# Kernel optimization log

Measured on AMD Instinct MI355X. Metric: run time of the kernel, lower is better.

The kernel has to match this reference:

```python
import jax, jax.numpy as jnp
import numpy as np

B, N, C, DK, TOPK = 4, 4096, 256, 64, 8


def setup_inputs() -> dict:
    key = jax.random.key(0)
    k1, k2, k3 = jax.random.split(key, 3)
    x = jax.random.normal(k1, (B, N, C), dtype=jnp.float32)
    # nn.Linear(channels, d_k, bias=False) weights, stored as [C, DK] for x @ W
    W_q = jax.random.normal(k2, (C, DK), dtype=jnp.float32) * (C ** -0.5)
    W_k = jax.random.normal(k3, (C, DK), dtype=jnp.float32) * (C ** -0.5)
    return {"x": x, "W_q": W_q, "W_k": W_k, "top_k": TOPK}


def reference(x, W_q, W_k, top_k):
    d_k = W_q.shape[-1]
    scale = d_k ** -0.5
    Q = x @ W_q                                   # [B, N, DK]
    K = x @ W_k                                   # [B, N, DK]
    S = jnp.einsum('bnd,bmd->bnm', Q, K) * scale  # [B, N, N]
    _, topk_idx = jax.lax.top_k(S, top_k)         # [B, N, top_k]
    n = S.shape[-1]
    # scatter True at top-k column indices per row (mirrors torch scatter_)
    row_mask = lambda idx: jnp.zeros((n,), dtype=bool).at[idx].set(True)
    mask = jax.vmap(jax.vmap(row_mask))(topk_idx)  # [B, N, N] bool
    S_masked = jnp.where(mask, S, -jnp.inf)
    A = jax.nn.softmax(S_masked, axis=-1)
    return A
```

## Files before the change

### kernel.cpp

```cpp
#include <hip/hip_runtime.h>
#include <math.h>

#define NROW 16384
#define NCOL 4096
#define CDIM 256
#define DKDIM 64
#define SCALE 0.125f

typedef float v4f __attribute__((ext_vector_type(4)));
typedef __attribute__((ext_vector_type(8))) short short8v;
typedef __attribute__((ext_vector_type(4))) float f32x4;

__device__ __forceinline__ unsigned mono(float v) {
  unsigned u = __float_as_uint(v);
  unsigned s = (unsigned)(((int)u) >> 31);
  return u ^ (s | 0x80000000u);
}
__device__ __forceinline__ float unmono(unsigned k) {
  unsigned u = (k & 0x80000000u) ? (k ^ 0x80000000u) : ~k;
  return __uint_as_float(u);
}
__device__ __forceinline__ unsigned short f2bf(float f) {
  unsigned u = __float_as_uint(f);
  u += 0x7FFFu + ((u >> 16) & 1u);
  return (unsigned short)(u >> 16);
}
__device__ __forceinline__ unsigned umaxu(unsigned a, unsigned b) { return a > b ? a : b; }

__device__ __forceinline__ void ins8(unsigned tk[8], unsigned& tmin, int& tmpos, unsigned v) {
  #pragma unroll
  for (int j = 0; j < 8; ++j) if (j == tmpos) tk[j] = v;
  tmin = tk[0]; tmpos = 0;
  #pragma unroll
  for (int j = 1; j < 8; ++j) if (tk[j] < tmin) { tmin = tk[j]; tmpos = j; }
}
__device__ __forceinline__ unsigned umax8(const unsigned kv[8]) {
  unsigned a = umaxu(umaxu(kv[0], kv[1]), umaxu(kv[2], kv[3]));
  unsigned b = umaxu(umaxu(kv[4], kv[5]), umaxu(kv[6], kv[7]));
  return umaxu(a, b);
}
__device__ __forceinline__ void seed8r(const unsigned kv[8],
                                       unsigned tk[8], unsigned& tmin, int& tmpos) {
  #pragma unroll
  for (int j = 0; j < 8; ++j) tk[j] = kv[j];
  tmin = tk[0]; tmpos = 0;
  #pragma unroll
  for (int j = 1; j < 8; ++j) if (tk[j] < tmin) { tmin = tk[j]; tmpos = j; }
}
__device__ __forceinline__ void scan8r(const unsigned kvin[8],
                                       unsigned tk[8], unsigned& tmin, int& tmpos) {
  unsigned kv[8];
  #pragma unroll
  for (int j = 0; j < 8; ++j) kv[j] = kvin[j];
  unsigned gm = umax8(kv);
  #pragma unroll
  for (int pass = 0; pass < 2; ++pass) {
    if (__any(gm > tmin)) {
      if (gm > tmin) {
        ins8(tk, tmin, tmpos, gm);
        #pragma unroll
        for (int j = 0; j < 8; ++j) if (kv[j] == gm) kv[j] = 0u;
      }
      gm = umax8(kv);
    }
  }
  if (__any(gm > tmin)) {
    #pragma unroll
    for (int j = 0; j < 8; ++j) if (kv[j] > tmin) ins8(tk, tmin, tmpos, kv[j]);
  }
}
__device__ __forceinline__ void seed8(const unsigned* __restrict__ sp,
                                      unsigned tk[8], unsigned& tmin, int& tmpos) {
  uint4 ka = *(const uint4*)(sp);
  uint4 kb = *(const uint4*)(sp + 4);
  unsigned kv[8] = {ka.x, ka.y, ka.z, ka.w, kb.x, kb.y, kb.z, kb.w};
  seed8r(kv, tk, tmin, tmpos);
}
__device__ __forceinline__ void scan8(const unsigned* __restrict__ sp,
                                      unsigned tk[8], unsigned& tmin, int& tmpos) {
  uint4 ka = *(const uint4*)(sp);
  uint4 kb = *(const uint4*)(sp + 4);
  unsigned kv[8] = {ka.x, ka.y, ka.z, ka.w, kb.x, kb.y, kb.z, kb.w};
  scan8r(kv, tk, tmin, tmpos);
}

__global__ __launch_bounds__(512, 2) void qk_proj(
    const float* __restrict__ x, const float* __restrict__ Wq,
    const float* __restrict__ Wk, float* __restrict__ Qt,
    float* __restrict__ Kt, unsigned short* __restrict__ Qh,
    unsigned short* __restrict__ Kh, float* __restrict__ out) {
  __shared__ float4 xs4[64][65];
  const int t = threadIdx.x;
  const int rb = blockIdx.x;
  {
    const float4* xg = (const float4*)(x + (size_t)rb * 64 * CDIM);
    #pragma unroll
    for (int i = 0; i < 8; ++i) {
      int idx = i * 512 + t;
      xs4[idx >> 6][idx & 63] = xg[idx];
    }
  }
  __syncthreads();

  const int lane = t & 63;
  const int wu = __builtin_amdgcn_readfirstlane(t >> 6);
  const int proj = wu >> 2;
  const int chunk = wu & 3;
  const float* __restrict__ Wp = proj ? Wk : Wq;

  v4f* __restrict__ ofill = (v4f*)out + (size_t)rb * 65536;
  const v4f z = {0.f, 0.f, 0.f, 0.f};

  float acc[16];
  #pragma unroll
  for (int j = 0; j < 16; ++j) acc[j] = 0.f;

  #pragma unroll 4
  for (int cs = 0; cs < 64; ++cs) {
    {
      int g0 = cs * 1024 + t;
      __builtin_nontemporal_store(z, &ofill[g0]);
      __builtin_nontemporal_store(z, &ofill[g0 + 512]);
    }
    float4 xv = xs4[lane][cs];
    const float xc[4] = {xv.x, xv.y, xv.z, xv.w};
    #pragma unroll
    for (int i = 0; i < 4; ++i) {
      const float4* __restrict__ w4 =
          (const float4*)(Wp + (size_t)(cs * 4 + i) * DKDIM + chunk * 16);
      float4 wa = w4[0], wb = w4[1], wc = w4[2], wd = w4[3];
      float xi = xc[i];
      acc[0]  = fmaf(xi, wa.x, acc[0]);  acc[1]  = fmaf(xi, wa.y, acc[1]);
      acc[2]  = fmaf(xi, wa.z, acc[2]);  acc[3]  = fmaf(xi, wa.w, acc[3]);
      acc[4]  = fmaf(xi, wb.x, acc[4]);  acc[5]  = fmaf(xi, wb.y, acc[5]);
      acc[6]  = fmaf(xi, wb.z, acc[6]);  acc[7]  = fmaf(xi, wb.w, acc[7]);
      acc[8]  = fmaf(xi, wc.x, acc[8]);  acc[9]  = fmaf(xi, wc.y, acc[9]);
      acc[10] = fmaf(xi, wc.z, acc[10]); acc[11] = fmaf(xi, wc.w, acc[11]);
      acc[12] = fmaf(xi, wd.x, acc[12]); acc[13] = fmaf(xi, wd.y, acc[13]);
      acc[14] = fmaf(xi, wd.z, acc[14]); acc[15] = fmaf(xi, wd.w, acc[15]);
    }
  }

  const int gr = rb * 64 + lane;
  float* Of = (proj ? Kt : Qt) + (size_t)gr * 64 + chunk * 16;
  #pragma unroll
  for (int i = 0; i < 4; ++i) {
    float4 o = {acc[4 * i], acc[4 * i + 1], acc[4 * i + 2], acc[4 * i + 3]};
    ((float4*)Of)[i] = o;
  }
  unsigned short* Oh = (proj ? Kh : Qh) + (size_t)gr * 64 + chunk * 16;
  unsigned hp[8];
  #pragma unroll
  for (int i = 0; i < 8; ++i)
    hp[i] = (unsigned)f2bf(acc[2 * i]) | ((unsigned)f2bf(acc[2 * i + 1]) << 16);
  uint4 h0 = {hp[0], hp[1], hp[2], hp[3]};
  uint4 h1 = {hp[4], hp[5], hp[6], hp[7]};
  ((uint4*)Oh)[0] = h0;
  ((uint4*)Oh)[1] = h1;
}

__global__ __launch_bounds__(256, 4) void s_cand(
    const unsigned short* __restrict__ Qh, const unsigned short* __restrict__ Kh,
    unsigned* __restrict__ wsk) {
  __shared__ unsigned keys[4][16 * 132];
  const int t = threadIdx.x;
  const int lane = t & 63;
  const int w = __builtin_amdgcn_readfirstlane(t >> 6);
  const int f = blockIdx.x;
  const int xs = f & 7;
  const int i5 = f >> 3;
  const int combo = xs * 4 + (i5 >> 6);
  const int rbL = i5 & 63;
  const int b = combo >> 3;
  const int chunk = combo & 7;

  const int l15 = lane & 15, lk = lane >> 4;
  const int rowg = (b << 12) + rbL * 64 + w * 16 + l15;
  const short8v a0 = *(const short8v*)(Qh + (size_t)rowg * 64 + lk * 8);
  const short8v a1 = *(const short8v*)(Qh + (size_t)rowg * 64 + lk * 8 + 32);

  const unsigned short* Kb = Kh + ((size_t)(b << 12)) * 64;

  unsigned tk[4][8]; unsigned tmin[4]; int tmpos[4];

  #pragma unroll 1
  for (int g = 0; g < 4; ++g) {
    unsigned kv[4][8];
    #pragma unroll
    for (int t8 = 0; t8 < 8; ++t8) {
      const int ct = g * 8 + t8;
      const int col = chunk * 512 + ct * 16 + l15;
      const unsigned short* kp = Kb + (size_t)col * 64 + lk * 8;
      const short8v b0 = *(const short8v*)(kp);
      const short8v b1 = *(const short8v*)(kp + 32);
      f32x4 acc = {0.f, 0.f, 0.f, 0.f};
      acc = __builtin_amdgcn_mfma_f32_16x16x32_bf16(a0, b0, acc, 0, 0, 0);
      acc = __builtin_amdgcn_mfma_f32_16x16x32_bf16(a1, b1, acc, 0, 0, 0);
      #pragma unroll
      for (int i = 0; i < 4; ++i)
        kv[i][t8] = (mono(acc[i]) & 0xFFFFF000u) | (unsigned)col;
    }
    if (g == 0) {
      #pragma unroll
      for (int i = 0; i < 4; ++i) seed8r(kv[i], tk[i], tmin[i], tmpos[i]);
    } else {
      #pragma unroll
      for (int i = 0; i < 4; ++i) scan8r(kv[i], tk[i], tmin[i], tmpos[i]);
    }
  }

  unsigned* krow = keys[w];
  #pragma unroll
  for (int i = 0; i < 4; ++i) {
    uint4 s0 = {tk[i][0], tk[i][1], tk[i][2], tk[i][3]};
    uint4 s1 = {tk[i][4], tk[i][5], tk[i][6], tk[i][7]};
    uint4* mp4 = (uint4*)(krow + (lk * 4 + i) * 132 + l15 * 8);
    mp4[0] = s0; mp4[1] = s1;
  }
  const int myrow = lane >> 2, q = lane & 3;
  unsigned mt[8]; unsigned mmin; int mmpos;
  {
    const unsigned* sp = krow + myrow * 132 + q * 32;
    seed8(sp, mt, mmin, mmpos);
    scan8(sp + 8, mt, mmin, mmpos);
    scan8(sp + 16, mt, mmin, mmpos);
    scan8(sp + 24, mt, mmin, mmpos);
  }
  {
    uint4 s0 = {mt[0], mt[1], mt[2], mt[3]};
    uint4 s1 = {mt[4], mt[5], mt[6], mt[7]};
    uint4* mp4 = (uint4*)(krow + myrow * 36 + q * 8);
    mp4[0] = s0; mp4[1] = s1;
  }
  if (lane < 16) {
    const unsigned* mp = krow + lane * 36;
    unsigned ft[8]; unsigned fmin; int fmpos;
    seed8(mp, ft, fmin, fmpos);
    scan8(mp + 8, ft, fmin, fmpos);
    scan8(mp + 16, ft, fmin, fmpos);
    scan8(mp + 24, ft, fmin, fmpos);
    const int grow = (b << 12) + rbL * 64 + w * 16 + lane;
    uint4 o0 = {ft[0], ft[1], ft[2], ft[3]};
    uint4 o1 = {ft[4], ft[5], ft[6], ft[7]};
    uint4* wp = (uint4*)(wsk + (size_t)grow * 64 + chunk * 8);
    wp[0] = o0; wp[1] = o1;
  }
}

__global__ __launch_bounds__(256) void finalize(
    const float* __restrict__ Qt, const float* __restrict__ Kt,
    const unsigned* __restrict__ wsk, float* __restrict__ out) {
  const int t = threadIdx.x;
  const int lane = t & 63;
  const int w = t >> 6;
  const int row = blockIdx.x * 4 + w;
  const int b = row >> 12;
  const unsigned key = wsk[(size_t)row * 64 + lane];
  const int col = (int)(key & 0xFFFu);
  const float4* Kp = (const float4*)(Kt + ((size_t)((b << 12) + col)) * 64);
  const float4* Qp = (const float4*)(Qt + (size_t)row * 64);
  float s = 0.f;
  #pragma unroll
  for (int g = 0; g < 16; ++g) {
    float4 qf = Qp[g];
    float4 kf = Kp[g];
    s = fmaf(qf.x, kf.x, s);
    s = fmaf(qf.y, kf.y, s);
    s = fmaf(qf.z, kf.z, s);
    s = fmaf(qf.w, kf.w, s);
  }
  unsigned kx = mono(s);
  float vals[8]; int cols[8];
  #pragma unroll
  for (int it = 0; it < 8; ++it) {
    unsigned m = kx;
    #pragma unroll
    for (int d = 1; d < 64; d <<= 1) m = umaxu(m, (unsigned)__shfl_xor((int)m, d, 64));
    unsigned long long win = __ballot(kx == m);
    int wl = (int)__ffsll(win) - 1;
    cols[it] = __shfl(col, wl, 64);
    vals[it] = unmono(m);
    if (lane == wl) kx = 0u;
  }
  float e[8], sum = 0.f;
  #pragma unroll
  for (int it = 0; it < 8; ++it) { e[it] = __expf((vals[it] - vals[0]) * SCALE); sum += e[it]; }
  float inv = 1.f / sum;
  if (lane == 0) {
    float* orow = out + ((size_t)row << 12);
    #pragma unroll
    for (int it = 0; it < 8; ++it) orow[cols[it]] = e[it] * inv;
  }
}

extern "C" void kernel_launch(void* const* d_in, const int* in_sizes, int n_in,
                              void* d_out, int out_size, void* d_ws, size_t ws_size,
                              hipStream_t stream) {
  const float* x  = (const float*)d_in[0];
  const float* Wq = (const float*)d_in[1];
  const float* Wk = (const float*)d_in[2];
  float* out = (float*)d_out;

  char* ws = (char*)d_ws;
  float* Qt = (float*)ws;
  float* Kt = (float*)(ws + ((size_t)4 << 20));
  unsigned short* Qh = (unsigned short*)(ws + ((size_t)8 << 20));
  unsigned short* Kh = (unsigned short*)(ws + ((size_t)10 << 20));
  unsigned* wsk = (unsigned*)(ws + ((size_t)12 << 20));

  qk_proj<<<dim3(NROW / 64), 512, 0, stream>>>(x, Wq, Wk, Qt, Kt, Qh, Kh, out);
  s_cand<<<2048, 256, 0, stream>>>(Qh, Kh, wsk);
  finalize<<<NROW / 4, 256, 0, stream>>>(Qt, Kt, wsk, out);
}
```

Before: 510.0 us.

## Move output zero-fill from projection kernel into finalize row writes

Before, the projection kernel zero-filled the whole 256MB output with nontemporal stores and finalize then scattered the 8 softmax values per row. Now finalize writes each complete row in one pass: every lane builds float4 chunks that are zero except at the top-k columns and stores them nontemporally. This removes the separate scattered writes and the second touch of those cache lines, and takes the fill traffic out of the projection kernel. In exchange, finalize becomes bound by output bandwidth, with extra compare/select work per element.

```diff
diff --git a/kernel.cpp b/kernel.cpp
--- a/kernel.cpp
+++ b/kernel.cpp
@@ -88,7 +88,7 @@
     const float* __restrict__ x, const float* __restrict__ Wq,
     const float* __restrict__ Wk, float* __restrict__ Qt,
     float* __restrict__ Kt, unsigned short* __restrict__ Qh,
-    unsigned short* __restrict__ Kh, float* __restrict__ out) {
+    unsigned short* __restrict__ Kh) {
   __shared__ float4 xs4[64][65];
   const int t = threadIdx.x;
   const int rb = blockIdx.x;
@@ -108,20 +108,12 @@
   const int chunk = wu & 3;
   const float* __restrict__ Wp = proj ? Wk : Wq;
 
-  v4f* __restrict__ ofill = (v4f*)out + (size_t)rb * 65536;
-  const v4f z = {0.f, 0.f, 0.f, 0.f};
-
   float acc[16];
   #pragma unroll
   for (int j = 0; j < 16; ++j) acc[j] = 0.f;
 
   #pragma unroll 4
   for (int cs = 0; cs < 64; ++cs) {
-    {
-      int g0 = cs * 1024 + t;
-      __builtin_nontemporal_store(z, &ofill[g0]);
-      __builtin_nontemporal_store(z, &ofill[g0 + 512]);
-    }
     float4 xv = xs4[lane][cs];
     const float xc[4] = {xv.x, xv.y, xv.z, xv.w};
     #pragma unroll
@@ -282,14 +274,26 @@
     vals[it] = unmono(m);
     if (lane == wl) kx = 0u;
   }
-  float e[8], sum = 0.f;
-  #pragma unroll
-  for (int it = 0; it < 8; ++it) { e[it] = __expf((vals[it] - vals[0]) * SCALE); sum += e[it]; }
+  float vq[8]; float sum = 0.f;
+  #pragma unroll
+  for (int it = 0; it < 8; ++it) { vq[it] = __expf((vals[it] - vals[0]) * SCALE); sum += vq[it]; }
   float inv = 1.f / sum;
-  if (lane == 0) {
-    float* orow = out + ((size_t)row << 12);
-    #pragma unroll
-    for (int it = 0; it < 8; ++it) orow[cols[it]] = e[it] * inv;
+  #pragma unroll
+  for (int it = 0; it < 8; ++it) vq[it] *= inv;
+
+  v4f* orow4 = (v4f*)(out + ((size_t)row << 12));
+  #pragma unroll
+  for (int i = 0; i < 16; ++i) {
+    const int base = i * 256 + lane * 4;
+    v4f z = {0.f, 0.f, 0.f, 0.f};
+    #pragma unroll
+    for (int q = 0; q < 8; ++q) {
+      z.x = (cols[q] == base)     ? vq[q] : z.x;
+      z.y = (cols[q] == base + 1) ? vq[q] : z.y;
+      z.z = (cols[q] == base + 2) ? vq[q] : z.z;
+      z.w = (cols[q] == base + 3) ? vq[q] : z.w;
+    }
+    __builtin_nontemporal_store(z, &orow4[(size_t)i * 64 + lane]);
   }
 }
 
@@ -308,7 +312,7 @@
   unsigned short* Kh = (unsigned short*)(ws + ((size_t)10 << 20));
   unsigned* wsk = (unsigned*)(ws + ((size_t)12 << 20));
 
-  qk_proj<<<dim3(NROW / 64), 512, 0, stream>>>(x, Wq, Wk, Qt, Kt, Qh, Kh, out);
+  qk_proj<<<dim3(NROW / 64), 512, 0, stream>>>(x, Wq, Wk, Qt, Kt, Qh, Kh);
   s_cand<<<2048, 256, 0, stream>>>(Qh, Kh, wsk);
   finalize<<<NROW / 4, 256, 0, stream>>>(Qt, Kt, wsk, out);
 }
```

After: 469.2 us. -8.0%, faster.
